# Performance work log

Measured on AMD Instinct MI355X. Metric: run time of the kernel, lower is better.

Reference implementation:

```python
import jax, jax.numpy as jnp
import numpy as np

N = 100000   # product nodes
E = 300000   # edges per relation
DIN = 128    # node_feature_dim
H = 128      # hidden_dim
NEG_SLOPE = 0.2


def setup_inputs() -> dict:
    key = jax.random.key(0)
    ks = iter(jax.random.split(key, 64))
    def nrm(shape, scale):
        return (jax.random.normal(next(ks), shape) * scale).astype(jnp.float32)
    d = {}
    d["x"] = nrm((N, DIN), 1.0)
    d["pos"] = nrm((N, 3), 1.0)
    for name in ("ei_chem", "ei_cond", "ei_mol"):
        d[name] = jax.random.randint(next(ks), (2, E), 0, N, dtype=jnp.int32)
    s = 1.0 / np.sqrt(H)
    d["Wp"] = nrm((DIN, H), 1.0 / np.sqrt(DIN)); d["bp"] = jnp.zeros((H,), jnp.float32)
    for L in ("1", "2"):
        for r in ("c", "d"):  # chemical_transformation, condition_modulation: heads=2
            d[f"W{L}{r}"] = nrm((H, H), s)
            d[f"as{L}{r}"] = nrm((2, H // 2), s)
            d[f"ad{L}{r}"] = nrm((2, H // 2), s)
            d[f"b{L}{r}"] = jnp.zeros((H,), jnp.float32)
        # molecule_target (EQGAT): heads=4
        d[f"W{L}m"] = nrm((H, H), s)
        d[f"as{L}m"] = nrm((4, H // 4), s)
        d[f"ad{L}m"] = nrm((4, H // 4), s)
        d[f"b{L}m"] = jnp.zeros((H,), jnp.float32)
        d[f"Wl{L}"] = nrm((H, H), s)
        d[f"bl{L}"] = jnp.zeros((H,), jnp.float32)
    d["Wy"] = nrm((H, 1), s); d["by"] = jnp.zeros((1,), jnp.float32)
    d["Wa"] = nrm((H, 1), s); d["ba"] = jnp.zeros((1,), jnp.float32)
    return d


def gat_conv(x, row, col, W, a_s, a_d, bias, heads, n):
    """PyG-style GATConv (concat=True, add_self_loops=True)."""
    Fh = W.shape[1] // heads
    loops = jnp.arange(n, dtype=row.dtype)
    row = jnp.concatenate([row, loops])
    col = jnp.concatenate([col, loops])
    h = (x @ W).reshape(n, heads, Fh)                      # [n,Hd,Fh]
    alpha_s = jnp.einsum('nhf,hf->nh', h, a_s)             # [n,Hd]
    alpha_d = jnp.einsum('nhf,hf->nh', h, a_d)
    e = jax.nn.leaky_relu(alpha_s[row] + alpha_d[col], NEG_SLOPE)  # [E',Hd]
    m = jax.lax.stop_gradient(jax.ops.segment_max(e, col, num_segments=n))
    ex = jnp.exp(e - m[col])
    z = jax.ops.segment_sum(ex, col, num_segments=n)
    alpha = ex / (z[col] + 1e-16)                          # per-dst softmax
    msg = h[row] * alpha[:, :, None]                       # [E',Hd,Fh]
    out = jax.ops.segment_sum(msg, col, num_segments=n).reshape(n, heads * Fh)
    return out + bias


def eqgat(x, pos, row, col, W, a_s, a_d, bias, Wl, bl, heads, n):
    geo = jnp.sqrt(jnp.sum((pos[row] - pos[col]) ** 2, axis=-1))  # [E]
    x = x + 0.1 * geo.mean()                                       # scalar broadcast
    h = gat_conv(x, row, col, W, a_s, a_d, bias, heads, n)
    return h @ Wl + bl


def reference(x, pos, ei_chem, ei_cond, ei_mol,
              Wp, bp,
              W1c, as1c, ad1c, b1c, W1d, as1d, ad1d, b1d,
              W1m, as1m, ad1m, b1m, Wl1, bl1,
              W2c, as2c, ad2c, b2c, W2d, as2d, ad2d, b2d,
              W2m, as2m, ad2m, b2m, Wl2, bl2,
              Wy, by, Wa, ba):
    n = x.shape[0]
    h0 = x @ Wp + bp
    h1 = jax.nn.relu(
        gat_conv(h0, ei_chem[0], ei_chem[1], W1c, as1c, ad1c, b1c, 2, n)
        + gat_conv(h0, ei_cond[0], ei_cond[1], W1d, as1d, ad1d, b1d, 2, n)
        + eqgat(h0, pos, ei_mol[0], ei_mol[1], W1m, as1m, ad1m, b1m, Wl1, bl1, 4, n))
    h2 = jax.nn.relu(
        gat_conv(h1, ei_chem[0], ei_chem[1], W2c, as2c, ad2c, b2c, 2, n)
        + gat_conv(h1, ei_cond[0], ei_cond[1], W2d, as2d, ad2d, b2d, 2, n)
        + eqgat(h1, pos, ei_mol[0], ei_mol[1], W2m, as2m, ad2m, b2m, Wl2, bl2, 4, n))
    pred_yield = (h2 @ Wy + by).squeeze(-1)
    pred_activity = (h2 @ Wa + ba).squeeze(-1)
    return jnp.stack([pred_yield, pred_activity], axis=-1)  # [n,2]
```

## Files before the change

### kernel.cpp

```cpp
#include <hip/hip_runtime.h>
#include <math.h>

typedef short short8 __attribute__((ext_vector_type(8)));
typedef float f32x4 __attribute__((ext_vector_type(4)));
typedef unsigned short us4 __attribute__((ext_vector_type(4)));

#define MAXDEG 32
#define GF_BIAS   1
#define GF_CSHIFT 2
#define GF_ALPHA  4
#define GF_BF16   8
#define NFRAG 18432

__device__ __forceinline__ unsigned short f2bf(float f) {
  unsigned u = __float_as_uint(f);
  u += 0x7FFF + ((u >> 16) & 1);
  return (unsigned short)(u >> 16);
}
__device__ __forceinline__ float bf2f(unsigned short s) { return __uint_as_float(((unsigned)s) << 16); }
__device__ __forceinline__ float lrelu(float v) { return v > 0.f ? v : 0.2f * v; }

__global__ __launch_bounds__(256) void k_scatter3(
    const int* __restrict__ ei0, const int* __restrict__ ei1, const int* __restrict__ ei2,
    int* __restrict__ cur,
    int* __restrict__ s0, int* __restrict__ s1, int* __restrict__ s2,
    const float* __restrict__ pos, float* __restrict__ gsum, int E, int N) {
  __shared__ float part[4];
  const int T4 = gridDim.x * 256;
  const int t = blockIdx.x * 256 + threadIdx.x;
  float d = 0.f;
  #pragma unroll
  for (int k = 0; k < 4; ++k) {
    const int idx = t + k * T4;
    if (idx >= 3 * E) continue;
    int rel, e;
    if (idx < E)          { rel = 0; e = idx; }
    else if (idx < 2 * E) { rel = 1; e = idx - E; }
    else                  { rel = 2; e = idx - 2 * E; }
    const int* ei = (rel == 0) ? ei0 : (rel == 1) ? ei1 : ei2;
    int* srcs     = (rel == 0) ? s0  : (rel == 1) ? s1  : s2;
    const int r = ei[e];
    const int c = ei[E + e];
    const int slot = atomicAdd(&cur[rel * N + c], 1);
    if (slot < MAXDEG) srcs[(size_t)c * MAXDEG + slot] = r;
    if (rel == 2) {
      const float dx = pos[3*r]   - pos[3*c];
      const float dy = pos[3*r+1] - pos[3*c+1];
      const float dz = pos[3*r+2] - pos[3*c+2];
      d += sqrtf(dx*dx + dy*dy + dz*dz);
    }
  }
  #pragma unroll
  for (int o = 32; o; o >>= 1) d += __shfl_down(d, o);
  if ((threadIdx.x & 63) == 0) part[threadIdx.x >> 6] = d;
  __syncthreads();
  if (threadIdx.x == 0) {
    const float s = part[0] + part[1] + part[2] + part[3];
    if (s != 0.f) atomicAdd(gsum, s);
  }
}

struct PrepArgs {
  const float* W[9];
  const float* as_[9];
  const float* ad_[9];
  unsigned short* hi[9];
  unsigned short* lo[9];
  float* csum[9];
  int fh[9];
};

__global__ __launch_bounds__(256) void k_prep(PrepArgs p) {
  const int s = blockIdx.x;
  const int t = threadIdx.x;
  const float* W = p.W[s];
  const int fh = p.fh[s];
  __shared__ float Ws[128 * 129];
  __shared__ float alpha[128 * 8];
  {
    const f32x4* src = (const f32x4*)W;
    for (int i = t; i < 4096; i += 256) {
      const f32x4 v = src[i];
      const int row = i >> 5;
      const int col = (i & 31) * 4;
      float* dst = &Ws[row * 129 + col];
      dst[0] = v[0]; dst[1] = v[1]; dst[2] = v[2]; dst[3] = v[3];
    }
  }
  __syncthreads();
  if (t < 128) {
    #pragma unroll
    for (int a = 0; a < 8; ++a) alpha[t * 8 + a] = 0.f;
    if (fh) {
      const int nh = 128 / fh;
      for (int h = 0; h < nh; ++h) {
        float s1 = 0.f, s2 = 0.f;
        for (int c = 0; c < fh; ++c) {
          const float w = Ws[t * 129 + h * fh + c];
          s1 += w * p.as_[s][h * fh + c];
          s2 += w * p.ad_[s][h * fh + c];
        }
        alpha[t * 8 + h] = s1;
        alpha[t * 8 + 4 + h] = s2;
      }
    }
  }
  __syncthreads();
  for (int idx = t; idx < NFRAG; idx += 256) {
    const int j = idx & 7, lane = (idx >> 3) & 63, kt = (idx >> 9) & 3, nt = idx >> 11;
    const int k = kt * 32 + (lane >> 4) * 8 + j;
    const int col = nt * 16 + (lane & 15);
    float w;
    if (col < 128) w = Ws[k * 129 + col];
    else if (col < 136) w = alpha[k * 8 + (col - 128)];
    else w = 0.f;
    const unsigned short h = f2bf(w);
    p.hi[s][idx] = h;
    p.lo[s][idx] = f2bf(w - bf2f(h));
  }
  if (t < 136) {
    float cs = 0.f;
    if (t < 128) for (int k = 0; k < 128; ++k) cs += Ws[k * 129 + t];
    else         for (int k = 0; k < 128; ++k) cs += alpha[k * 8 + (t - 128)];
    p.csum[s][t] = cs;
  }
}

__global__ __launch_bounds__(256, 2) void k_gmm(
    const float* __restrict__ A, const unsigned short* __restrict__ Whi,
    const unsigned short* __restrict__ Wlo, const float* __restrict__ csum,
    const float* __restrict__ bias, float* __restrict__ C,
    float* __restrict__ aS, float* __restrict__ aD,
    const float* __restrict__ gsum, float gscale,
    int n, int npad, int flags)
{
  __shared__ unsigned short shi[NFRAG];
  __shared__ unsigned short slo[NFRAG];
  {
    const f32x4* srch = (const f32x4*)Whi;
    const f32x4* srcl = (const f32x4*)Wlo;
    f32x4* dsth = (f32x4*)shi;
    f32x4* dstl = (f32x4*)slo;
    for (int i = threadIdx.x; i < NFRAG / 8; i += 256) { dsth[i] = srch[i]; dstl[i] = srcl[i]; }
  }
  __syncthreads();

  const int wave = threadIdx.x >> 6, lane = threadIdx.x & 63;
  const int m = lane & 15, kq = lane >> 4;
  const float cb = (flags & GF_CSHIFT) ? gscale * gsum[0] : 0.f;

  for (int rb = blockIdx.x * 128; rb < npad; rb += gridDim.x * 128) {
    const int rw = rb + wave * 32;
    short8 ah[2][4], al[2][4];
    #pragma unroll
    for (int sub = 0; sub < 2; ++sub) {
      const int row = rw + sub * 16 + m;
      const bool ok = row < n;
      const float* ap = A + (size_t)row * 128 + kq * 8;
      #pragma unroll
      for (int kt = 0; kt < 4; ++kt) {
        f32x4 x0 = {0.f, 0.f, 0.f, 0.f}, x1 = {0.f, 0.f, 0.f, 0.f};
        if (ok) { x0 = *(const f32x4*)(ap + kt * 32); x1 = *(const f32x4*)(ap + kt * 32 + 4); }
        #pragma unroll
        for (int j = 0; j < 4; ++j) {
          unsigned short h0 = f2bf(x0[j]);
          ah[sub][kt][j] = (short)h0;
          al[sub][kt][j] = (short)f2bf(x0[j] - bf2f(h0));
          unsigned short h1 = f2bf(x1[j]);
          ah[sub][kt][4 + j] = (short)h1;
          al[sub][kt][4 + j] = (short)f2bf(x1[j] - bf2f(h1));
        }
      }
    }
    f32x4 acc[2][9];
    #pragma unroll
    for (int sub = 0; sub < 2; ++sub)
      #pragma unroll
      for (int nt = 0; nt < 9; ++nt) acc[sub][nt] = f32x4{0.f, 0.f, 0.f, 0.f};

    #pragma unroll
    for (int nt = 0; nt < 9; ++nt) {
      #pragma unroll
      for (int kt = 0; kt < 4; ++kt) {
        const int fo = ((nt * 4 + kt) * 64 + lane) * 8;
        const short8 bh = *(const short8*)&shi[fo];
        const short8 bl = *(const short8*)&slo[fo];
        #pragma unroll
        for (int sub = 0; sub < 2; ++sub) {
          acc[sub][nt] = __builtin_amdgcn_mfma_f32_16x16x32_bf16(ah[sub][kt], bh, acc[sub][nt], 0, 0, 0);
          acc[sub][nt] = __builtin_amdgcn_mfma_f32_16x16x32_bf16(al[sub][kt], bh, acc[sub][nt], 0, 0, 0);
          acc[sub][nt] = __builtin_amdgcn_mfma_f32_16x16x32_bf16(ah[sub][kt], bl, acc[sub][nt], 0, 0, 0);
        }
      }
    }
    #pragma unroll
    for (int sub = 0; sub < 2; ++sub) {
      const int rbase = rw + sub * 16 + kq * 4;
      #pragma unroll
      for (int nt = 0; nt < 8; ++nt) {
        const int col = nt * 16 + m;
        const float cs = (flags & GF_CSHIFT) ? cb * csum[col] : 0.f;
        const float bb = (flags & GF_BIAS) ? bias[col] : 0.f;
        if (flags & GF_BF16) {
          unsigned short* Cb = (unsigned short*)C;
          #pragma unroll
          for (int r = 0; r < 4; ++r)
            Cb[(size_t)(rbase + r) * 128 + col] = f2bf(acc[sub][nt][r] + cs);
        } else {
          #pragma unroll
          for (int r = 0; r < 4; ++r)
            C[(size_t)(rbase + r) * 128 + col] = acc[sub][nt][r] + cs + bb;
        }
      }
      if ((flags & GF_ALPHA) && m < 8) {
        const float cs = (flags & GF_CSHIFT) ? cb * csum[128 + m] : 0.f;
        #pragma unroll
        for (int r = 0; r < 4; ++r) {
          const float v = acc[sub][8][r] + cs;
          const int row = rbase + r;
          if (m < 4) aS[(size_t)row * 4 + m] = v;
          else       aD[(size_t)row * 4 + (m - 4)] = v;
        }
      }
    }
  }
}

__global__ __launch_bounds__(256) void k_conv(
    const unsigned short* __restrict__ hb, const float* __restrict__ aS,
    const float* __restrict__ aD,
    const int* __restrict__ srcs, const int* __restrict__ cnt,
    const float* __restrict__ bias, float* __restrict__ out,
    int fh_shift, int mode, int n)
{
  __shared__ int   ssh[4][2][32];
  __shared__ float wsh[4][2][32][4];
  const int wv = threadIdx.x >> 6;
  const int lane = threadIdx.x & 63;
  const int hf = lane >> 5;
  const int l  = lane & 31;
  const int i = blockIdx.x * 8 + wv * 2 + hf;
  const bool iok = i < n;
  const int ipad = iok ? i : 0;
  const int c0 = l * 4;
  const int hd = c0 >> fh_shift;

  int deg = 0;
  if (iok) { deg = cnt[i]; if (deg > MAXDEG) deg = MAXDEG; }
  const int* sp = srcs + (size_t)ipad * MAXDEG;

  const bool valid = l < deg;
  int s = ipad;
  if (valid) s = sp[l];

  f32x4 ad4 = f32x4{0.f, 0.f, 0.f, 0.f}, asi = f32x4{0.f, 0.f, 0.f, 0.f};
  if (iok) {
    ad4 = *(const f32x4*)(aD + (size_t)i * 4);
    asi = *(const f32x4*)(aS + (size_t)i * 4);
  }
  f32x4 as4 = f32x4{0.f, 0.f, 0.f, 0.f};
  if (valid) as4 = *(const f32x4*)(aS + (size_t)s * 4);

  f32x4 e, eself;
  #pragma unroll
  for (int hh = 0; hh < 4; ++hh) {
    e[hh] = lrelu(as4[hh] + ad4[hh]);
    eself[hh] = lrelu(asi[hh] + ad4[hh]);
  }

  f32x4 mx;
  #pragma unroll
  for (int hh = 0; hh < 4; ++hh) mx[hh] = valid ? e[hh] : -1e30f;
  #pragma unroll
  for (int o = 16; o; o >>= 1) {
    #pragma unroll
    for (int hh = 0; hh < 4; ++hh) mx[hh] = fmaxf(mx[hh], __shfl_xor(mx[hh], o, 32));
  }
  #pragma unroll
  for (int hh = 0; hh < 4; ++hh) mx[hh] = fmaxf(mx[hh], eself[hh]);

  f32x4 w, z;
  #pragma unroll
  for (int hh = 0; hh < 4; ++hh) { w[hh] = valid ? __expf(e[hh] - mx[hh]) : 0.f; z[hh] = w[hh]; }
  #pragma unroll
  for (int o = 16; o; o >>= 1) {
    #pragma unroll
    for (int hh = 0; hh < 4; ++hh) z[hh] += __shfl_xor(z[hh], o, 32);
  }
  f32x4 wsf;
  #pragma unroll
  for (int hh = 0; hh < 4; ++hh) { wsf[hh] = __expf(eself[hh] - mx[hh]); z[hh] += wsf[hh]; }

  int dtot = (deg + 3) & ~3;
  const int dmax = max(dtot, __shfl_xor(dtot, 32));
  if (l < dmax) {
    ssh[wv][hf][l] = valid ? s : ipad;
    f32x4 wst = f32x4{0.f, 0.f, 0.f, 0.f};
    if (valid) wst = w;
    *(f32x4*)wsh[wv][hf][l] = wst;
  }

  f32x4 acc = f32x4{0.f, 0.f, 0.f, 0.f};
  {
    us4 u = {0, 0, 0, 0};
    if (iok) u = *(const us4*)(hb + (size_t)i * 128 + c0);
    const float ws = wsf[hd];
    #pragma unroll
    for (int q = 0; q < 4; ++q) acc[q] = ws * bf2f(u[q]);
  }
  for (int j0 = 0; j0 < dmax; j0 += 4) {
    const int s0 = ssh[wv][hf][j0],     s1 = ssh[wv][hf][j0 + 1];
    const int s2 = ssh[wv][hf][j0 + 2], s3 = ssh[wv][hf][j0 + 3];
    const float w0 = wsh[wv][hf][j0][hd],     w1 = wsh[wv][hf][j0 + 1][hd];
    const float w2 = wsh[wv][hf][j0 + 2][hd], w3 = wsh[wv][hf][j0 + 3][hd];
    const us4 u0 = *(const us4*)(hb + (size_t)s0 * 128 + c0);
    const us4 u1 = *(const us4*)(hb + (size_t)s1 * 128 + c0);
    const us4 u2 = *(const us4*)(hb + (size_t)s2 * 128 + c0);
    const us4 u3 = *(const us4*)(hb + (size_t)s3 * 128 + c0);
    #pragma unroll
    for (int q = 0; q < 4; ++q)
      acc[q] += w0 * bf2f(u0[q]) + w1 * bf2f(u1[q]) + w2 * bf2f(u2[q]) + w3 * bf2f(u3[q]);
  }

  if (!iok) return;
  const float inv = 1.f / (z[hd] + 1e-16f);
  const f32x4 bb = *(const f32x4*)(bias + c0);
  float* op = out + (size_t)i * 128 + c0;
  f32x4 res;
  #pragma unroll
  for (int q = 0; q < 4; ++q) res[q] = acc[q] * inv + bb[q];
  if (mode == 0) { *(f32x4*)op = res; }
  else {
    f32x4 cur = *(const f32x4*)op;
    #pragma unroll
    for (int q = 0; q < 4; ++q) {
      float r = cur[q] + res[q];
      if (mode == 2) r = fmaxf(r, 0.f);
      res[q] = r;
    }
    *(f32x4*)op = res;
  }
}

__global__ __launch_bounds__(256) void k_conv2(
    const unsigned short* __restrict__ hcp, const unsigned short* __restrict__ hdp,
    const float* __restrict__ aSc, const float* __restrict__ aDc,
    const float* __restrict__ aSd, const float* __restrict__ aDd,
    const int* __restrict__ srcs_c, const int* __restrict__ cnt_c,
    const int* __restrict__ srcs_d, const int* __restrict__ cnt_d,
    const float* __restrict__ bias_c, const float* __restrict__ bias_d,
    float* __restrict__ out, int fh_shift, int n)
{
  __shared__ int   ssh[4][2][2][32];
  __shared__ float wsh[4][2][2][32][4];
  const int wv = threadIdx.x >> 6;
  const int lane = threadIdx.x & 63;
  const int hf = lane >> 5;
  const int l  = lane & 31;
  const int i = blockIdx.x * 8 + wv * 2 + hf;
  const bool iok = i < n;
  const int ipad = iok ? i : 0;
  const int c0 = l * 4;
  const int hd = c0 >> fh_shift;

  const unsigned short* hA[2] = {hcp, hdp};
  const float* aSA[2]  = {aSc, aSd};
  const float* aDA[2]  = {aDc, aDd};
  const int*   spA[2]  = {srcs_c, srcs_d};
  const int*   cntA[2] = {cnt_c, cnt_d};

  int deg[2]; bool valid[2]; int s[2];
  f32x4 ad4[2], asi[2], as4[2];
  #pragma unroll
  for (int r = 0; r < 2; ++r) {
    deg[r] = 0;
    if (iok) { int d = cntA[r][i]; deg[r] = d > MAXDEG ? MAXDEG : d; }
  }
  #pragma unroll
  for (int r = 0; r < 2; ++r) {
    const int* sp = spA[r] + (size_t)ipad * MAXDEG;
    valid[r] = l < deg[r];
    s[r] = valid[r] ? sp[l] : ipad;
  }
  #pragma unroll
  for (int r = 0; r < 2; ++r) {
    ad4[r] = f32x4{0.f, 0.f, 0.f, 0.f};
    asi[r] = f32x4{0.f, 0.f, 0.f, 0.f};
    if (iok) {
      ad4[r] = *(const f32x4*)(aDA[r] + (size_t)i * 4);
      asi[r] = *(const f32x4*)(aSA[r] + (size_t)i * 4);
    }
  }
  #pragma unroll
  for (int r = 0; r < 2; ++r) {
    as4[r] = f32x4{0.f, 0.f, 0.f, 0.f};
    if (valid[r]) as4[r] = *(const f32x4*)(aSA[r] + (size_t)s[r] * 4);
  }

  f32x4 e[2], eself[2], mx[2];
  #pragma unroll
  for (int r = 0; r < 2; ++r)
    #pragma unroll
    for (int hh = 0; hh < 4; ++hh) {
      e[r][hh] = lrelu(as4[r][hh] + ad4[r][hh]);
      eself[r][hh] = lrelu(asi[r][hh] + ad4[r][hh]);
      mx[r][hh] = valid[r] ? e[r][hh] : -1e30f;
    }
  #pragma unroll
  for (int o = 16; o; o >>= 1)
    #pragma unroll
    for (int r = 0; r < 2; ++r)
      #pragma unroll
      for (int hh = 0; hh < 4; ++hh)
        mx[r][hh] = fmaxf(mx[r][hh], __shfl_xor(mx[r][hh], o, 32));
  f32x4 w[2], z[2];
  #pragma unroll
  for (int r = 0; r < 2; ++r)
    #pragma unroll
    for (int hh = 0; hh < 4; ++hh) {
      mx[r][hh] = fmaxf(mx[r][hh], eself[r][hh]);
      w[r][hh] = valid[r] ? __expf(e[r][hh] - mx[r][hh]) : 0.f;
      z[r][hh] = w[r][hh];
    }
  #pragma unroll
  for (int o = 16; o; o >>= 1)
    #pragma unroll
    for (int r = 0; r < 2; ++r)
      #pragma unroll
      for (int hh = 0; hh < 4; ++hh)
        z[r][hh] += __shfl_xor(z[r][hh], o, 32);
  f32x4 wsf[2], inv[2];
  #pragma unroll
  for (int r = 0; r < 2; ++r)
    #pragma unroll
    for (int hh = 0; hh < 4; ++hh) {
      wsf[r][hh] = __expf(eself[r][hh] - mx[r][hh]);
      z[r][hh] += wsf[r][hh];
      inv[r][hh] = 1.f / (z[r][hh] + 1e-16f);
    }

  f32x4 acc = f32x4{0.f, 0.f, 0.f, 0.f};
  #pragma unroll
  for (int rel = 0; rel < 2; ++rel) {
    int dtot = (deg[rel] + 3) & ~3;
    const int dmax = max(dtot, __shfl_xor(dtot, 32));
    if (l < dmax) {
      ssh[wv][rel][hf][l] = valid[rel] ? s[rel] : ipad;
      f32x4 wst = f32x4{0.f, 0.f, 0.f, 0.f};
      if (valid[rel]) {
        #pragma unroll
        for (int hh = 0; hh < 4; ++hh) wst[hh] = w[rel][hh] * inv[rel][hh];
      }
      *(f32x4*)wsh[wv][rel][hf][l] = wst;
    }

    const unsigned short* hmat = hA[rel];
    {
      us4 u = {0, 0, 0, 0};
      if (iok) u = *(const us4*)(hmat + (size_t)i * 128 + c0);
      const float ws = wsf[rel][hd] * inv[rel][hd];
      #pragma unroll
      for (int q = 0; q < 4; ++q) acc[q] += ws * bf2f(u[q]);
    }
    for (int j0 = 0; j0 < dmax; j0 += 4) {
      const int s0 = ssh[wv][rel][hf][j0],     s1 = ssh[wv][rel][hf][j0 + 1];
      const int s2 = ssh[wv][rel][hf][j0 + 2], s3 = ssh[wv][rel][hf][j0 + 3];
      const float w0 = wsh[wv][rel][hf][j0][hd],     w1 = wsh[wv][rel][hf][j0 + 1][hd];
      const float w2 = wsh[wv][rel][hf][j0 + 2][hd], w3 = wsh[wv][rel][hf][j0 + 3][hd];
      const us4 u0 = *(const us4*)(hmat + (size_t)s0 * 128 + c0);
      const us4 u1 = *(const us4*)(hmat + (size_t)s1 * 128 + c0);
      const us4 u2 = *(const us4*)(hmat + (size_t)s2 * 128 + c0);
      const us4 u3 = *(const us4*)(hmat + (size_t)s3 * 128 + c0);
      #pragma unroll
      for (int q = 0; q < 4; ++q)
        acc[q] += w0 * bf2f(u0[q]) + w1 * bf2f(u1[q]) + w2 * bf2f(u2[q]) + w3 * bf2f(u3[q]);
    }
  }

  if (!iok) return;
  const f32x4 bbc = *(const f32x4*)(bias_c + c0);
  const f32x4 bbd = *(const f32x4*)(bias_d + c0);
  float* op = out + (size_t)i * 128 + c0;
  const f32x4 cur = *(const f32x4*)op;
  f32x4 res;
  #pragma unroll
  for (int q = 0; q < 4; ++q)
    res[q] = fmaxf(cur[q] + acc[q] + bbc[q] + bbd[q], 0.f);
  *(f32x4*)op = res;
}

__global__ __launch_bounds__(256) void k_head(
    const float* __restrict__ h2, const float* __restrict__ Wy, const float* __restrict__ by,
    const float* __restrict__ Wa, const float* __restrict__ ba,
    float* __restrict__ out, int n)
{
  const int r = blockIdx.x * 4 + (threadIdx.x >> 6);
  const int L = threadIdx.x & 63;
  if (r >= n) return;
  const float a = h2[(size_t)r * 128 + L];
  const float b = h2[(size_t)r * 128 + 64 + L];
  float py = a * Wy[L] + b * Wy[64 + L];
  float pa = a * Wa[L] + b * Wa[64 + L];
  #pragma unroll
  for (int o = 32; o; o >>= 1) { py += __shfl_down(py, o); pa += __shfl_down(pa, o); }
  if (L == 0) {
    out[(size_t)r * 2]     = py + by[0];
    out[(size_t)r * 2 + 1] = pa + ba[0];
  }
}

extern "C" void kernel_launch(void* const* d_in, const int* in_sizes, int n_in,
                              void* d_out, int out_size, void* d_ws, size_t ws_size,
                              hipStream_t stream) {
  const int N = in_sizes[0] / 128;
  const int E = in_sizes[2] / 2;
  const int npad = (N + 127) & ~127;

  const float* x       = (const float*)d_in[0];
  const float* pos     = (const float*)d_in[1];
  const int*   ei_chem = (const int*)d_in[2];
  const int*   ei_cond = (const int*)d_in[3];
  const int*   ei_mol  = (const int*)d_in[4];
  const float* bp = (const float*)d_in[6];
  const float* Wy = (const float*)d_in[35];
  const float* by = (const float*)d_in[36];
  const float* Wa = (const float*)d_in[37];
  const float* ba = (const float*)d_in[38];

  char* ws = (char*)d_ws;
  size_t off = 0;
  auto alloc = [&](size_t bytes) -> void* {
    void* p = ws + off; off += (bytes + 255) & ~(size_t)255; return p;
  };
  const size_t HB = (size_t)npad * 128 * sizeof(float);
  const size_t HBH = (size_t)npad * 128 * sizeof(unsigned short);
  float* H0  = (float*)alloc(HB);
  float* ACC = (float*)alloc(HB);
  unsigned short* HRb  = (unsigned short*)alloc(HBH);
  unsigned short* HRb2 = (unsigned short*)alloc(HBH);
  int* SRC[3];
  for (int r = 0; r < 3; ++r) SRC[r] = (int*)alloc((size_t)N * MAXDEG * sizeof(int));
  int*   CUR  = (int*)alloc((size_t)3 * N * sizeof(int));
  float* GSUM = (float*)alloc(256);
  float* AS   = (float*)alloc((size_t)npad * 4 * sizeof(float));
  float* AD   = (float*)alloc((size_t)npad * 4 * sizeof(float));
  float* ASd  = (float*)alloc((size_t)npad * 4 * sizeof(float));
  float* ADd  = (float*)alloc((size_t)npad * 4 * sizeof(float));

  PrepArgs pa{};
  const int widx[9] = {5, 7, 11, 15, 19, 21, 25, 29, 33};
  const int fhs[9]  = {0, 64, 64, 32, 0, 64, 64, 32, 0};
  unsigned short *WHI[9], *WLO[9];
  float* CSUM[9];
  for (int s = 0; s < 9; ++s) {
    WHI[s]  = (unsigned short*)alloc(NFRAG * sizeof(unsigned short));
    WLO[s]  = (unsigned short*)alloc(NFRAG * sizeof(unsigned short));
    CSUM[s] = (float*)alloc(144 * sizeof(float));
    pa.W[s] = (const float*)d_in[widx[s]];
    pa.fh[s] = fhs[s];
    pa.as_[s] = fhs[s] ? (const float*)d_in[widx[s] + 1] : nullptr;
    pa.ad_[s] = fhs[s] ? (const float*)d_in[widx[s] + 2] : nullptr;
    pa.hi[s] = WHI[s]; pa.lo[s] = WLO[s]; pa.csum[s] = CSUM[s];
  }

  hipMemsetAsync(CUR, 0, (size_t)3 * N * sizeof(int), stream);
  hipMemsetAsync(GSUM, 0, sizeof(float), stream);

  {
    const int nthreads = (3 * E + 3) / 4;
    const int sgrid = (nthreads + 255) / 256;
    k_scatter3<<<sgrid, 256, 0, stream>>>(ei_chem, ei_cond, ei_mol,
                                          CUR, SRC[0], SRC[1], SRC[2],
                                          pos, GSUM, E, N);
  }
  k_prep<<<9, 256, 0, stream>>>(pa);

  const int GG = 512;
  const float gscale = 0.1f / (float)E;
  const int cgrid = (N + 7) / 8;

  k_gmm<<<GG, 256, 0, stream>>>(x, WHI[0], WLO[0], CSUM[0], bp, H0,
                                nullptr, nullptr, nullptr, 0.f, N, npad, GF_BIAS);

  auto layer = [&](const float* Hin, float* Acc, int base, int s0) {
    const float* bc = (const float*)d_in[base + 3];
    const float* bd = (const float*)d_in[base + 7];
    const float* bm = (const float*)d_in[base + 11];
    const float* bl = (const float*)d_in[base + 13];
    k_gmm<<<GG, 256, 0, stream>>>(Hin, WHI[s0+2], WLO[s0+2], CSUM[s0+2], nullptr,
                                  (float*)HRb, AS, AD, GSUM, gscale, N, npad,
                                  GF_CSHIFT | GF_ALPHA | GF_BF16);
    k_conv<<<cgrid, 256, 0, stream>>>(HRb, AS, AD, SRC[2], CUR + 2*N, bm, Acc, 5, 0, N);
    k_gmm<<<GG, 256, 0, stream>>>(Acc, WHI[s0+3], WLO[s0+3], CSUM[s0+3], bl, Acc,
                                  nullptr, nullptr, nullptr, 0.f, N, npad, GF_BIAS);
    k_gmm<<<GG, 256, 0, stream>>>(Hin, WHI[s0+0], WLO[s0+0], CSUM[s0+0], nullptr,
                                  (float*)HRb, AS, AD, nullptr, 0.f, N, npad,
                                  GF_ALPHA | GF_BF16);
    k_gmm<<<GG, 256, 0, stream>>>(Hin, WHI[s0+1], WLO[s0+1], CSUM[s0+1], nullptr,
                                  (float*)HRb2, ASd, ADd, nullptr, 0.f, N, npad,
                                  GF_ALPHA | GF_BF16);
    k_conv2<<<cgrid, 256, 0, stream>>>(HRb, HRb2, AS, AD, ASd, ADd,
                                       SRC[0], CUR + 0*N, SRC[1], CUR + 1*N,
                                       bc, bd, Acc, 6, N);
  };

  layer(H0, ACC, 7, 1);
  layer(ACC, H0, 21, 5);

  k_head<<<(N + 3) / 4, 256, 0, stream>>>(H0, Wy, by, Wa, ba, (float*)d_out, N);
}
```

Baseline: 771.1 us.

## Store all intermediate activations in bf16 and add bf16-input GEMM kernel

Hidden activations H0 and the accumulator buffer change from fp32 to bf16 across the GEMM, conv, conv2 and head kernels. A new k_gmmb kernel reads bf16 activations directly, which cuts the A-side split to two MFMA passes (hi-A with hi-W and lo-W) instead of three. This halves activation memory traffic and removes a third of the MFMA work in most GEMMs, at the cost of bf16 rounding error on the stored activations and on the accumulated layer outputs.

```diff
diff --git a/kernel.cpp b/kernel.cpp
--- a/kernel.cpp
+++ b/kernel.cpp
@@ -9,7 +9,6 @@
 #define GF_BIAS   1
 #define GF_CSHIFT 2
 #define GF_ALPHA  4
-#define GF_BF16   8
 #define NFRAG 18432
 
 __device__ __forceinline__ unsigned short f2bf(float f) {
@@ -129,7 +128,7 @@
 __global__ __launch_bounds__(256, 2) void k_gmm(
     const float* __restrict__ A, const unsigned short* __restrict__ Whi,
     const unsigned short* __restrict__ Wlo, const float* __restrict__ csum,
-    const float* __restrict__ bias, float* __restrict__ C,
+    const float* __restrict__ bias, unsigned short* __restrict__ C,
     float* __restrict__ aS, float* __restrict__ aD,
     const float* __restrict__ gsum, float gscale,
     int n, int npad, int flags)
@@ -201,16 +200,9 @@
         const int col = nt * 16 + m;
         const float cs = (flags & GF_CSHIFT) ? cb * csum[col] : 0.f;
         const float bb = (flags & GF_BIAS) ? bias[col] : 0.f;
-        if (flags & GF_BF16) {
-          unsigned short* Cb = (unsigned short*)C;
-          #pragma unroll
-          for (int r = 0; r < 4; ++r)
-            Cb[(size_t)(rbase + r) * 128 + col] = f2bf(acc[sub][nt][r] + cs);
-        } else {
-          #pragma unroll
-          for (int r = 0; r < 4; ++r)
-            C[(size_t)(rbase + r) * 128 + col] = acc[sub][nt][r] + cs + bb;
-        }
+        #pragma unroll
+        for (int r = 0; r < 4; ++r)
+          C[(size_t)(rbase + r) * 128 + col] = f2bf(acc[sub][nt][r] + cs + bb);
       }
       if ((flags & GF_ALPHA) && m < 8) {
         const float cs = (flags & GF_CSHIFT) ? cb * csum[128 + m] : 0.f;
@@ -226,12 +218,95 @@
   }
 }
 
+__global__ __launch_bounds__(256, 2) void k_gmmb(
+    const unsigned short* __restrict__ A, const unsigned short* __restrict__ Whi,
+    const unsigned short* __restrict__ Wlo, const float* __restrict__ csum,
+    const float* __restrict__ bias, unsigned short* __restrict__ C,
+    float* __restrict__ aS, float* __restrict__ aD,
+    const float* __restrict__ gsum, float gscale,
+    int n, int npad, int flags)
+{
+  __shared__ unsigned short shi[NFRAG];
+  __shared__ unsigned short slo[NFRAG];
+  {
+    const f32x4* srch = (const f32x4*)Whi;
+    const f32x4* srcl = (const f32x4*)Wlo;
+    f32x4* dsth = (f32x4*)shi;
+    f32x4* dstl = (f32x4*)slo;
+    for (int i = threadIdx.x; i < NFRAG / 8; i += 256) { dsth[i] = srch[i]; dstl[i] = srcl[i]; }
+  }
+  __syncthreads();
+
+  const int wave = threadIdx.x >> 6, lane = threadIdx.x & 63;
+  const int m = lane & 15, kq = lane >> 4;
+  const float cb = (flags & GF_CSHIFT) ? gscale * gsum[0] : 0.f;
+
+  for (int rb = blockIdx.x * 128; rb < npad; rb += gridDim.x * 128) {
+    const int rw = rb + wave * 32;
+    short8 ah[2][4];
+    #pragma unroll
+    for (int sub = 0; sub < 2; ++sub) {
+      const int row = rw + sub * 16 + m;
+      const bool ok = row < n;
+      const unsigned short* ap = A + (size_t)row * 128 + kq * 8;
+      #pragma unroll
+      for (int kt = 0; kt < 4; ++kt) {
+        if (ok) ah[sub][kt] = *(const short8*)(ap + kt * 32);
+        else    ah[sub][kt] = short8{0, 0, 0, 0, 0, 0, 0, 0};
+      }
+    }
+    f32x4 acc[2][9];
+    #pragma unroll
+    for (int sub = 0; sub < 2; ++sub)
+      #pragma unroll
+      for (int nt = 0; nt < 9; ++nt) acc[sub][nt] = f32x4{0.f, 0.f, 0.f, 0.f};
+
+    #pragma unroll
+    for (int nt = 0; nt < 9; ++nt) {
+      #pragma unroll
+      for (int kt = 0; kt < 4; ++kt) {
+        const int fo = ((nt * 4 + kt) * 64 + lane) * 8;
+        const short8 bh = *(const short8*)&shi[fo];
+        const short8 bl = *(const short8*)&slo[fo];
+        #pragma unroll
+        for (int sub = 0; sub < 2; ++sub) {
+          acc[sub][nt] = __builtin_amdgcn_mfma_f32_16x16x32_bf16(ah[sub][kt], bh, acc[sub][nt], 0, 0, 0);
+          acc[sub][nt] = __builtin_amdgcn_mfma_f32_16x16x32_bf16(ah[sub][kt], bl, acc[sub][nt], 0, 0, 0);
+        }
+      }
+    }
+    #pragma unroll
+    for (int sub = 0; sub < 2; ++sub) {
+      const int rbase = rw + sub * 16 + kq * 4;
+      #pragma unroll
+      for (int nt = 0; nt < 8; ++nt) {
+        const int col = nt * 16 + m;
+        const float cs = (flags & GF_CSHIFT) ? cb * csum[col] : 0.f;
+        const float bb = (flags & GF_BIAS) ? bias[col] : 0.f;
+        #pragma unroll
+        for (int r = 0; r < 4; ++r)
+          C[(size_t)(rbase + r) * 128 + col] = f2bf(acc[sub][nt][r] + cs + bb);
+      }
+      if ((flags & GF_ALPHA) && m < 8) {
+        const float cs = (flags & GF_CSHIFT) ? cb * csum[128 + m] : 0.f;
+        #pragma unroll
+        for (int r = 0; r < 4; ++r) {
+          const float v = acc[sub][8][r] + cs;
+          const int row = rbase + r;
+          if (m < 4) aS[(size_t)row * 4 + m] = v;
+          else       aD[(size_t)row * 4 + (m - 4)] = v;
+        }
+      }
+    }
+  }
+}
+
 __global__ __launch_bounds__(256) void k_conv(
     const unsigned short* __restrict__ hb, const float* __restrict__ aS,
     const float* __restrict__ aD,
     const int* __restrict__ srcs, const int* __restrict__ cnt,
-    const float* __restrict__ bias, float* __restrict__ out,
-    int fh_shift, int mode, int n)
+    const float* __restrict__ bias, unsigned short* __restrict__ out,
+    int fh_shift, int n)
 {
   __shared__ int   ssh[4][2][32];
   __shared__ float wsh[4][2][32][4];
@@ -325,21 +400,11 @@
   if (!iok) return;
   const float inv = 1.f / (z[hd] + 1e-16f);
   const f32x4 bb = *(const f32x4*)(bias + c0);
-  float* op = out + (size_t)i * 128 + c0;
-  f32x4 res;
-  #pragma unroll
-  for (int q = 0; q < 4; ++q) res[q] = acc[q] * inv + bb[q];
-  if (mode == 0) { *(f32x4*)op = res; }
-  else {
-    f32x4 cur = *(const f32x4*)op;
-    #pragma unroll
-    for (int q = 0; q < 4; ++q) {
-      float r = cur[q] + res[q];
-      if (mode == 2) r = fmaxf(r, 0.f);
-      res[q] = r;
-    }
-    *(f32x4*)op = res;
-  }
+  unsigned short* op = out + (size_t)i * 128 + c0;
+  us4 res;
+  #pragma unroll
+  for (int q = 0; q < 4; ++q) res[q] = f2bf(acc[q] * inv + bb[q]);
+  *(us4*)op = res;
 }
 
 __global__ __launch_bounds__(256) void k_conv2(
@@ -349,7 +414,7 @@
     const int* __restrict__ srcs_c, const int* __restrict__ cnt_c,
     const int* __restrict__ srcs_d, const int* __restrict__ cnt_d,
     const float* __restrict__ bias_c, const float* __restrict__ bias_d,
-    float* __restrict__ out, int fh_shift, int n)
+    unsigned short* __restrict__ out, int fh_shift, int n)
 {
   __shared__ int   ssh[4][2][2][32];
   __shared__ float wsh[4][2][2][32][4];
@@ -480,25 +545,26 @@
   if (!iok) return;
   const f32x4 bbc = *(const f32x4*)(bias_c + c0);
   const f32x4 bbd = *(const f32x4*)(bias_d + c0);
-  float* op = out + (size_t)i * 128 + c0;
-  const f32x4 cur = *(const f32x4*)op;
-  f32x4 res;
+  unsigned short* op = out + (size_t)i * 128 + c0;
+  const us4 cu = *(const us4*)op;
+  us4 res;
   #pragma unroll
   for (int q = 0; q < 4; ++q)
-    res[q] = fmaxf(cur[q] + acc[q] + bbc[q] + bbd[q], 0.f);
-  *(f32x4*)op = res;
+    res[q] = f2bf(fmaxf(bf2f(cu[q]) + acc[q] + bbc[q] + bbd[q], 0.f));
+  *(us4*)op = res;
 }
 
 __global__ __launch_bounds__(256) void k_head(
-    const float* __restrict__ h2, const float* __restrict__ Wy, const float* __restrict__ by,
+    const unsigned short* __restrict__ h2, const float* __restrict__ Wy,
+    const float* __restrict__ by,
     const float* __restrict__ Wa, const float* __restrict__ ba,
     float* __restrict__ out, int n)
 {
   const int r = blockIdx.x * 4 + (threadIdx.x >> 6);
   const int L = threadIdx.x & 63;
   if (r >= n) return;
-  const float a = h2[(size_t)r * 128 + L];
-  const float b = h2[(size_t)r * 128 + 64 + L];
+  const float a = bf2f(h2[(size_t)r * 128 + L]);
+  const float b = bf2f(h2[(size_t)r * 128 + 64 + L]);
   float py = a * Wy[L] + b * Wy[64 + L];
   float pa = a * Wa[L] + b * Wa[64 + L];
   #pragma unroll
@@ -532,10 +598,9 @@
   auto alloc = [&](size_t bytes) -> void* {
     void* p = ws + off; off += (bytes + 255) & ~(size_t)255; return p;
   };
-  const size_t HB = (size_t)npad * 128 * sizeof(float);
   const size_t HBH = (size_t)npad * 128 * sizeof(unsigned short);
-  float* H0  = (float*)alloc(HB);
-  float* ACC = (float*)alloc(HB);
+  unsigned short* H0b  = (unsigned short*)alloc(HBH);
+  unsigned short* ACCb = (unsigned short*)alloc(HBH);
   unsigned short* HRb  = (unsigned short*)alloc(HBH);
   unsigned short* HRb2 = (unsigned short*)alloc(HBH);
   int* SRC[3];
@@ -579,33 +644,31 @@
   const float gscale = 0.1f / (float)E;
   const int cgrid = (N + 7) / 8;
 
-  k_gmm<<<GG, 256, 0, stream>>>(x, WHI[0], WLO[0], CSUM[0], bp, H0,
+  k_gmm<<<GG, 256, 0, stream>>>(x, WHI[0], WLO[0], CSUM[0], bp, H0b,
                                 nullptr, nullptr, nullptr, 0.f, N, npad, GF_BIAS);
 
-  auto layer = [&](const float* Hin, float* Acc, int base, int s0) {
+  auto layer = [&](const unsigned short* Hin, unsigned short* Acc, int base, int s0) {
     const float* bc = (const float*)d_in[base + 3];
     const float* bd = (const float*)d_in[base + 7];
     const float* bm = (const float*)d_in[base + 11];
     const float* bl = (const float*)d_in[base + 13];
-    k_gmm<<<GG, 256, 0, stream>>>(Hin, WHI[s0+2], WLO[s0+2], CSUM[s0+2], nullptr,
-                                  (float*)HRb, AS, AD, GSUM, gscale, N, npad,
-                                  GF_CSHIFT | GF_ALPHA | GF_BF16);
-    k_conv<<<cgrid, 256, 0, stream>>>(HRb, AS, AD, SRC[2], CUR + 2*N, bm, Acc, 5, 0, N);
-    k_gmm<<<GG, 256, 0, stream>>>(Acc, WHI[s0+3], WLO[s0+3], CSUM[s0+3], bl, Acc,
-                                  nullptr, nullptr, nullptr, 0.f, N, npad, GF_BIAS);
-    k_gmm<<<GG, 256, 0, stream>>>(Hin, WHI[s0+0], WLO[s0+0], CSUM[s0+0], nullptr,
-                                  (float*)HRb, AS, AD, nullptr, 0.f, N, npad,
-                                  GF_ALPHA | GF_BF16);
-    k_gmm<<<GG, 256, 0, stream>>>(Hin, WHI[s0+1], WLO[s0+1], CSUM[s0+1], nullptr,
-                                  (float*)HRb2, ASd, ADd, nullptr, 0.f, N, npad,
-                                  GF_ALPHA | GF_BF16);
+    k_gmmb<<<GG, 256, 0, stream>>>(Hin, WHI[s0+2], WLO[s0+2], CSUM[s0+2], nullptr,
+                                   HRb, AS, AD, GSUM, gscale, N, npad,
+                                   GF_CSHIFT | GF_ALPHA);
+    k_conv<<<cgrid, 256, 0, stream>>>(HRb, AS, AD, SRC[2], CUR + 2*N, bm, Acc, 5, N);
+    k_gmmb<<<GG, 256, 0, stream>>>(Acc, WHI[s0+3], WLO[s0+3], CSUM[s0+3], bl, Acc,
+                                   nullptr, nullptr, nullptr, 0.f, N, npad, GF_BIAS);
+    k_gmmb<<<GG, 256, 0, stream>>>(Hin, WHI[s0+0], WLO[s0+0], CSUM[s0+0], nullptr,
+                                   HRb, AS, AD, nullptr, 0.f, N, npad, GF_ALPHA);
+    k_gmmb<<<GG, 256, 0, stream>>>(Hin, WHI[s0+1], WLO[s0+1], CSUM[s0+1], nullptr,
+                                   HRb2, ASd, ADd, nullptr, 0.f, N, npad, GF_ALPHA);
     k_conv2<<<cgrid, 256, 0, stream>>>(HRb, HRb2, AS, AD, ASd, ADd,
                                        SRC[0], CUR + 0*N, SRC[1], CUR + 1*N,
                                        bc, bd, Acc, 6, N);
   };
 
-  layer(H0, ACC, 7, 1);
-  layer(ACC, H0, 21, 5);
-
-  k_head<<<(N + 3) / 4, 256, 0, stream>>>(H0, Wy, by, Wa, ba, (float*)d_out, N);
-}
+  layer(H0b, ACCb, 7, 1);
+  layer(ACCb, H0b, 21, 5);
+
+  k_head<<<(N + 3) / 4, 256, 0, stream>>>(H0b, Wy, by, Wa, ba, (float*)d_out, N);
+}
```

After: 670.4 us. 1.15x faster.
